# Kernel optimization log

Measured on AMD Instinct MI355X. Metric: run time of the kernel, lower is better.

The kernel has to match this reference:

```python
import jax, jax.numpy as jnp
import numpy as np

B, Q, KL, ML, D = 2, 1024, 1024, 1024, 1024
H, DK = 16, 64  # adim = H*DK = 1024
SCALE = float(np.sqrt(DK))


def _rel_shift(x):
    # x: [B, qlen, klen, H] -> TransformerXL relative shift
    b, q, k, h = x.shape
    x = jnp.pad(x, ((0, 0), (0, 0), (1, 0), (0, 0)))  # [B,q,k+1,H]
    x = x.reshape(b, k + 1, q, h)[:, 1:]               # drop first row of shifted view
    return x.reshape(b, q, k, h)


def setup_inputs() -> dict:
    key = jax.random.key(0)
    ks = jax.random.split(key, 12)
    n = lambda i, s, scale=1.0: jax.random.normal(ks[i], s, jnp.float32) * scale
    return {
        "key_x": n(0, (B, KL, D)),
        "query": n(1, (B, Q, D)),
        "memory": n(2, (B, ML, D)),
        "pos_embs": n(3, (KL + ML, 1, D)),
        "mask": jnp.ones((B, Q, KL + ML), jnp.int32),
        "u": n(4, (H, DK), 0.02),
        "v": n(5, (H, DK), 0.02),
        "w_key": n(6, (D, H * DK), 0.02),
        "w_value": n(7, (D, H * DK), 0.02),
        "w_query": n(8, (D, H * DK), 0.02),
        "w_position": n(9, (D, H * DK), 0.02),
        "w_out": n(10, (H * DK, D), 0.02),
    }


def reference(key_x, query, memory, pos_embs, mask, u, v,
              w_key, w_value, w_query, w_position, w_out):
    bs, qlen = query.shape[:2]
    kv = jnp.concatenate([memory, key_x], axis=1)          # [B, mlen+klen, D]
    klen_tot = kv.shape[1]
    val = (kv @ w_value).reshape(bs, klen_tot, H, DK)
    k = (kv @ w_key).reshape(bs, klen_tot, H, DK)
    q = (query @ w_query).reshape(bs, qlen, H, DK)
    pos = (pos_embs.reshape(-1, pos_embs.shape[-1]) @ w_position).reshape(-1, H, DK)
    AC = jnp.einsum('bihd,bjhd->bijh', q + u[None, None], k)
    BD = jnp.einsum('bihd,jhd->bijh', q + v[None, None], pos)
    BD = _rel_shift(BD)
    e = (AC + BD) / SCALE                                   # [B, q, k, H]
    neg_inf = jnp.finfo(e.dtype).min
    e = jnp.where(mask[..., None] == 0, neg_inf, e)
    aw = jax.nn.softmax(e, axis=2)
    cv = jnp.einsum('bijh,bjhd->bihd', aw, val).reshape(bs, qlen, H * DK)
    cv = cv @ w_out
    return cv, aw.transpose(0, 3, 1, 2)
```

## Files before the change

### kernel.cpp

```cpp
#include <hip/hip_runtime.h>
#include <stdint.h>

#define H 16
#define DK 64
#define QL 1024
#define KT 2048
#define DM 1024
#define BATCH 2

typedef __attribute__((ext_vector_type(4))) float f32x4;
typedef __attribute__((ext_vector_type(8))) short s16x8;

enum { EPI_K = 0, EPI_V = 1, EPI_QUV = 2, EPI_P = 3, EPI_OUT = 4 };

__device__ __forceinline__ unsigned short f2bf(float f) {
  union { float f; uint32_t u; } v; v.f = f;
  uint32_t u = v.u;
  u += 0x7fffu + ((u >> 16) & 1u);
  return (unsigned short)(u >> 16);
}
__device__ __forceinline__ float bf2f(unsigned short s) {
  union { uint32_t u; float f; } v; v.u = ((uint32_t)s) << 16;
  return v.f;
}

#define MFMA_BF16(A, B, C) __builtin_amdgcn_mfma_f32_16x16x32_bf16((A), (B), (C), 0, 0, 0)

__device__ __forceinline__ void gld_lds16(const void* g, void* l) {
  __builtin_amdgcn_global_load_lds(
      (const __attribute__((address_space(1))) void*)g,
      (__attribute__((address_space(3))) void*)l, 16, 0, 0);
}


__global__ __launch_bounds__(256) void cast_kv_kernel(
    const float* __restrict__ mem, const float* __restrict__ keyx,
    unsigned short* __restrict__ kv) {
  size_t i4 = (size_t)blockIdx.x * blockDim.x + threadIdx.x;
  if (i4 >= (size_t)BATCH * KT * DM / 4) return;
  size_t e = i4 * 4;
  int b = (int)(e >> 21);
  int rem = (int)(e & ((1u << 21) - 1));
  int j = rem >> 10;
  int d = rem & 1023;
  const float* src = (j < 1024)
      ? (mem + ((size_t)b << 20) + ((size_t)j << 10) + d)
      : (keyx + ((size_t)b << 20) + ((size_t)(j - 1024) << 10) + d);
  float4 v = *(const float4*)src;
  ushort4 o;
  o.x = f2bf(v.x); o.y = f2bf(v.y); o.z = f2bf(v.z); o.w = f2bf(v.w);
  *(ushort4*)(kv + e) = o;
}

__global__ __launch_bounds__(256) void cast4_kernel(
    const float* __restrict__ src, unsigned short* __restrict__ dst, int n4) {
  int i4 = blockIdx.x * blockDim.x + threadIdx.x;
  if (i4 >= n4) return;
  float4 v = *(const float4*)(src + (size_t)i4 * 4);
  ushort4 o;
  o.x = f2bf(v.x); o.y = f2bf(v.y); o.z = f2bf(v.z); o.w = f2bf(v.w);
  *(ushort4*)(dst + (size_t)i4 * 4) = o;
}

__global__ __launch_bounds__(256) void transpose_cast_kernel(
    const float* __restrict__ w0, const float* __restrict__ w1,
    const float* __restrict__ w2, const float* __restrict__ w3,
    const float* __restrict__ w4,
    unsigned short* __restrict__ o0, unsigned short* __restrict__ o1,
    unsigned short* __restrict__ o2, unsigned short* __restrict__ o3,
    unsigned short* __restrict__ o4) {
  __shared__ float tile[32][33];
  const float* src; unsigned short* dst;
  switch (blockIdx.z) {
    case 0: src = w0; dst = o0; break;
    case 1: src = w1; dst = o1; break;
    case 2: src = w2; dst = o2; break;
    case 3: src = w3; dst = o3; break;
    default: src = w4; dst = o4; break;
  }
  int bx = blockIdx.x * 32, by = blockIdx.y * 32;
  int tx = threadIdx.x;
  int ty = threadIdx.y;
#pragma unroll
  for (int r = 0; r < 4; ++r)
    tile[ty + r * 8][tx] = src[(size_t)(by + ty + r * 8) * DM + bx + tx];
  __syncthreads();
#pragma unroll
  for (int r = 0; r < 4; ++r)
    dst[(size_t)(bx + ty + r * 8) * DM + by + tx] = f2bf(tile[tx][ty + r * 8]);
}

__global__ __launch_bounds__(256) void pack_mask_kernel(
    const int* __restrict__ mask, unsigned long long* __restrict__ bits) {
  int t = blockIdx.x * blockDim.x + threadIdx.x;
  int wid = t >> 6, lane = t & 63;
  int v = mask[(size_t)wid * 64 + lane];
  unsigned long long bb = __ballot(v != 0);
  if (lane == 0) bits[wid] = bb;
}


__global__ __launch_bounds__(256) void gemm_nt_kernel(
    const unsigned short* __restrict__ A, const unsigned short* __restrict__ B,
    int K, int mode,
    unsigned short* __restrict__ out0, unsigned short* __restrict__ out1,
    float* __restrict__ outf,
    const float* __restrict__ uvec, const float* __restrict__ vvec) {
  __shared__ __align__(16) unsigned short lds[128 * 64 * 2];
  char* As = (char*)lds;
  char* Bs = (char*)lds + 128 * 64 * 2;

  const int tid = threadIdx.x;
  const int w = tid >> 6, lane = tid & 63;
  const int g = lane >> 4, l15 = lane & 15;
  const int m0 = blockIdx.y * 128, n0 = blockIdx.x * 128;
  const int wm = w >> 1, wn = w & 1;

  f32x4 zf = {0.f, 0.f, 0.f, 0.f};
  f32x4 acc[4][4];
#pragma unroll
  for (int a = 0; a < 4; ++a)
#pragma unroll
    for (int c = 0; c < 4; ++c) acc[a][c] = zf;

  for (int kt = 0; kt < K; kt += 64) {
#pragma unroll
    for (int q = 0; q < 4; ++q) {
      int o = (w * 4 + q) * 1024 + lane * 16;
      int row = o >> 7;
      int slot = (o & 127) >> 4;
      int ks = slot ^ (row & 7);
      gld_lds16(A + (size_t)(m0 + row) * K + kt + ks * 8, As + o);
      gld_lds16(B + (size_t)(n0 + row) * K + kt + ks * 8, Bs + o);
    }
    asm volatile("s_waitcnt vmcnt(0)" ::: "memory");
    __syncthreads();
#pragma unroll
    for (int kk = 0; kk < 2; ++kk) {
      s16x8 af[4], bfr[4];
#pragma unroll
      for (int mf = 0; mf < 4; ++mf) {
        int row = wm * 64 + mf * 16 + l15;
        af[mf] = *(const s16x8*)(As + row * 128 + ((kk * 64 + g * 16) ^ ((row & 7) << 4)));
      }
#pragma unroll
      for (int nf = 0; nf < 4; ++nf) {
        int row = wn * 64 + nf * 16 + l15;
        bfr[nf] = *(const s16x8*)(Bs + row * 128 + ((kk * 64 + g * 16) ^ ((row & 7) << 4)));
      }
#pragma unroll
      for (int mf = 0; mf < 4; ++mf)
#pragma unroll
        for (int nf = 0; nf < 4; ++nf)
          acc[mf][nf] = MFMA_BF16(af[mf], bfr[nf], acc[mf][nf]);
    }
    __syncthreads();
  }

#pragma unroll
  for (int mf = 0; mf < 4; ++mf) {
#pragma unroll
    for (int nf = 0; nf < 4; ++nf) {
#pragma unroll
      for (int i = 0; i < 4; ++i) {
        int m = m0 + wm * 64 + mf * 16 + g * 4 + i;
        int n = n0 + wn * 64 + nf * 16 + l15;
        float val = acc[mf][nf][i];
        if (mode == EPI_K) {
          int b = m >> 11, j = m & 2047, hh = n >> 6, d = n & 63;
          out0[(((size_t)(b * H + hh) * KT + j) << 6) + d] = f2bf(val);
        } else if (mode == EPI_V) {
          int hh = m >> 6, d = m & 63, b = n >> 11, j = n & 2047;
          out0[((size_t)(b * H + hh) * 64 + d) * KT + j] = f2bf(val);
        } else if (mode == EPI_QUV) {
          int b = m >> 10, i2 = m & 1023, hh = n >> 6, d = n & 63;
          size_t idx = ((size_t)(b * H + hh) * QL + i2) * 64 + d;
          out0[idx] = f2bf(val + uvec[n]);
          out1[idx] = f2bf(val + vvec[n]);
        } else if (mode == EPI_P) {
          int hh = n >> 6, d = n & 63;
          out0[(((size_t)hh * KT + m) << 6) + d] = f2bf(val);
        } else {
          outf[(size_t)m * DM + n] = val;
        }
      }
    }
  }
}


__global__ __launch_bounds__(256) void attn_kernel(
    const unsigned short* __restrict__ Qu, const unsigned short* __restrict__ Qv,
    const unsigned short* __restrict__ Kp, const unsigned short* __restrict__ Vt,
    const unsigned short* __restrict__ Pp,
    const unsigned long long* __restrict__ mbits,
    float* __restrict__ aw, unsigned short* __restrict__ cv) {
  __shared__ __align__(16) unsigned short smem[12288];
  const int w = threadIdx.x >> 6, lane = threadIdx.x & 63;
  const int g = lane >> 4, l15 = lane & 15;
  const int b = blockIdx.z, h = blockIdx.y;
  const int r0 = blockIdx.x * 64 + w * 16;
  const int bh = b * H + h;

  const unsigned short* Qu_b = Qu + (size_t)bh * QL * 64;
  const unsigned short* Qv_b = Qv + (size_t)bh * QL * 64;
  const unsigned short* Kp_b = Kp + (size_t)bh * KT * 64;
  const unsigned short* Vt_b = Vt + (size_t)bh * 64 * KT;
  const unsigned short* Pp_b = Pp + (size_t)h * KT * 64;
  float* aw_b = aw + (size_t)bh * QL * KT;
  const unsigned long long* mb_b = mbits + (size_t)b * QL * 32;

  char* ring = (char*)smem + w * 4096;
  char* plds = (char*)smem + 16384 + w * 2048;

  s16x8 zv = {0, 0, 0, 0, 0, 0, 0, 0};
  s16x8 qu[2], qv[2], qvp[2];
  {
    int r = r0 + l15;
#pragma unroll
    for (int kk = 0; kk < 2; ++kk) {
      qu[kk] = *(const s16x8*)(Qu_b + (size_t)r * 64 + kk * 32 + g * 8);
      qv[kk] = *(const s16x8*)(Qv_b + (size_t)r * 64 + kk * 32 + g * 8);
    }
    int rp = r0 + 1 + l15;
    if (rp < QL) {
#pragma unroll
      for (int kk = 0; kk < 2; ++kk)
        qvp[kk] = *(const s16x8*)(Qv_b + (size_t)rp * 64 + kk * 32 + g * 8);
    } else {
      qvp[0] = zv; qvp[1] = zv;
    }
  }

  f32x4 zf = {0.f, 0.f, 0.f, 0.f};
  const int cfirst = (1008 - r0) >> 6;

  auto compute_chunk = [&](int c) {
    const int T = c << 6;
    const bool wrap = (T >= KT);
    f32x4 bd[4];
#pragma unroll
    for (int nf = 0; nf < 4; ++nf) bd[nf] = zf;
#pragma unroll
    for (int kk = 0; kk < 2; ++kk) {
      const s16x8 a = wrap ? qvp[kk] : qv[kk];
#pragma unroll
      for (int nf = 0; nf < 4; ++nf) {
        int t = T + nf * 16 + l15;
        int prow = wrap ? (t - (KT + 1)) : t;
        s16x8 pb = zv;
        if (prow >= 0 && prow < KT)
          pb = *(const s16x8*)(Pp_b + (size_t)prow * 64 + kk * 32 + g * 8);
        bd[nf] = MFMA_BF16(a, pb, bd[nf]);
      }
    }
    char* dst = ring + (c & 1) * 2048;
#pragma unroll
    for (int nf = 0; nf < 4; ++nf)
#pragma unroll
      for (int i = 0; i < 4; ++i) {
        int rr = g * 4 + i;
        *(unsigned short*)(dst + rr * 128 + (((nf * 16 + l15) * 2) ^ ((rr & 7) << 4))) =
            f2bf(bd[nf][i]);
      }
  };

  auto step_e = [&](int s, float (&e)[4][4]) {
    const int j0 = s * 64;
    compute_chunk(cfirst + 1 + s);
    f32x4 acc[4];
#pragma unroll
    for (int nf = 0; nf < 4; ++nf) acc[nf] = zf;
#pragma unroll
    for (int kk = 0; kk < 2; ++kk) {
#pragma unroll
      for (int nf = 0; nf < 4; ++nf) {
        int j = j0 + nf * 16 + l15;
        s16x8 kb = *(const s16x8*)(Kp_b + (size_t)j * 64 + kk * 32 + g * 8);
        acc[nf] = MFMA_BF16(qu[kk], kb, acc[nf]);
      }
    }
    asm volatile("s_waitcnt lgkmcnt(0)" ::: "memory");
#pragma unroll
    for (int i = 0; i < 4; ++i) {
      int rr = g * 4 + i;
      unsigned long long mw = mb_b[(size_t)(r0 + rr) * 32 + s];
#pragma unroll
      for (int nf = 0; nf < 4; ++nf) {
        int j = j0 + nf * 16 + l15;
        int t = j + 1023 - (r0 + rr);
        float bdv = bf2f(*(const unsigned short*)(
            ring + ((t >> 6) & 1) * 2048 + rr * 128 + (((t & 63) * 2) ^ ((rr & 7) << 4))));
        float ev = (acc[nf][i] + bdv) * 0.125f;
        ev = ((mw >> (j & 63)) & 1ull) ? ev : -1e30f;
        e[nf][i] = ev;
      }
    }
  };

  float mrow[4], lrow[4];
#pragma unroll
  for (int i = 0; i < 4; ++i) { mrow[i] = -1e30f; lrow[i] = 0.f; }

  compute_chunk(cfirst);
  for (int s = 0; s < 32; ++s) {
    float e[4][4];
    step_e(s, e);
#pragma unroll
    for (int i = 0; i < 4; ++i) {
      float tmax = fmaxf(fmaxf(e[0][i], e[1][i]), fmaxf(e[2][i], e[3][i]));
#pragma unroll
      for (int d2 = 8; d2 > 0; d2 >>= 1) tmax = fmaxf(tmax, __shfl_xor(tmax, d2));
      float mnew = fmaxf(mrow[i], tmax);
      float ssum = __expf(e[0][i] - mnew) + __expf(e[1][i] - mnew) +
                   __expf(e[2][i] - mnew) + __expf(e[3][i] - mnew);
#pragma unroll
      for (int d2 = 8; d2 > 0; d2 >>= 1) ssum += __shfl_xor(ssum, d2);
      lrow[i] = lrow[i] * __expf(mrow[i] - mnew) + ssum;
      mrow[i] = mnew;
    }
  }

  f32x4 accO[4];
#pragma unroll
  for (int df = 0; df < 4; ++df) accO[df] = zf;
  float rl[4];
#pragma unroll
  for (int i = 0; i < 4; ++i) rl[i] = 1.f / lrow[i];

  compute_chunk(cfirst);
  for (int s = 0; s < 32; ++s) {
    const int j0 = s * 64;
    float e[4][4];
    step_e(s, e);
#pragma unroll
    for (int i = 0; i < 4; ++i) {
      int rr = g * 4 + i;
#pragma unroll
      for (int nf = 0; nf < 4; ++nf) {
        float p = __expf(e[nf][i] - mrow[i]) * rl[i];
        int j = j0 + nf * 16 + l15;
        aw_b[(size_t)(r0 + rr) * KT + j] = p;
        *(unsigned short*)(plds + rr * 128 + (((nf * 16 + l15) * 2) ^ ((rr & 7) << 4))) = f2bf(p);
      }
    }
    asm volatile("s_waitcnt lgkmcnt(0)" ::: "memory");
#pragma unroll
    for (int kk = 0; kk < 2; ++kk) {
      s16x8 pa = *(const s16x8*)(plds + l15 * 128 + ((kk * 64 + g * 16) ^ ((l15 & 7) << 4)));
#pragma unroll
      for (int df = 0; df < 4; ++df) {
        int d = df * 16 + l15;
        s16x8 vb = *(const s16x8*)(Vt_b + (size_t)d * KT + j0 + kk * 32 + g * 8);
        accO[df] = MFMA_BF16(pa, vb, accO[df]);
      }
    }
  }

#pragma unroll
  for (int df = 0; df < 4; ++df)
#pragma unroll
    for (int i = 0; i < 4; ++i) {
      int r = r0 + g * 4 + i;
      int d = df * 16 + l15;
      cv[((size_t)b * QL + r) * DM + h * 64 + d] = f2bf(accO[df][i]);
    }
}


extern "C" void kernel_launch(void* const* d_in, const int* in_sizes, int n_in,
                              void* d_out, int out_size, void* d_ws, size_t ws_size,
                              hipStream_t stream) {
  const float* key_x  = (const float*)d_in[0];
  const float* query  = (const float*)d_in[1];
  const float* memory = (const float*)d_in[2];
  const float* pose   = (const float*)d_in[3];
  const int*   mask   = (const int*)d_in[4];
  const float* u      = (const float*)d_in[5];
  const float* v      = (const float*)d_in[6];
  const float* w_key  = (const float*)d_in[7];
  const float* w_val  = (const float*)d_in[8];
  const float* w_qry  = (const float*)d_in[9];
  const float* w_pos  = (const float*)d_in[10];
  const float* w_out  = (const float*)d_in[11];

  char* ws = (char*)d_ws;
  const size_t MB = 1024 * 1024;
  unsigned short* kv_b  = (unsigned short*)(ws + 0);
  unsigned short* q_b   = (unsigned short*)(ws + 8 * MB);
  unsigned short* pos_b = (unsigned short*)(ws + 12 * MB);
  unsigned short* wk_t  = (unsigned short*)(ws + 16 * MB);
  unsigned short* wv_t  = (unsigned short*)(ws + 18 * MB);
  unsigned short* wq_t  = (unsigned short*)(ws + 20 * MB);
  unsigned short* wp_t  = (unsigned short*)(ws + 22 * MB);
  unsigned short* wo_t  = (unsigned short*)(ws + 24 * MB);
  unsigned short* Kp    = (unsigned short*)(ws + 26 * MB);
  unsigned short* Vt    = (unsigned short*)(ws + 34 * MB);
  unsigned short* Qu    = (unsigned short*)(ws + 42 * MB);
  unsigned short* Qv    = (unsigned short*)(ws + 46 * MB);
  unsigned short* Pp    = (unsigned short*)(ws + 50 * MB);
  unsigned short* cvb   = (unsigned short*)(ws + 54 * MB);
  unsigned long long* mb = (unsigned long long*)(ws + 58 * MB);

  float* out_cv = (float*)d_out;
  float* out_aw = (float*)d_out + (size_t)BATCH * QL * DM;

  cast_kv_kernel<<<4096, 256, 0, stream>>>(memory, key_x, kv_b);
  cast4_kernel<<<2048, 256, 0, stream>>>(query, q_b, BATCH * QL * DM / 4);
  cast4_kernel<<<2048, 256, 0, stream>>>(pose, pos_b, KT * DM / 4);
  transpose_cast_kernel<<<dim3(32, 32, 5), dim3(32, 8), 0, stream>>>(
      w_key, w_val, w_qry, w_pos, w_out, wk_t, wv_t, wq_t, wp_t, wo_t);
  pack_mask_kernel<<<16384, 256, 0, stream>>>(mask, mb);

  gemm_nt_kernel<<<dim3(8, 32), 256, 0, stream>>>(kv_b, wk_t, 1024, EPI_K, Kp, nullptr, nullptr, nullptr, nullptr);
  gemm_nt_kernel<<<dim3(32, 8), 256, 0, stream>>>(wv_t, kv_b, 1024, EPI_V, Vt, nullptr, nullptr, nullptr, nullptr);
  gemm_nt_kernel<<<dim3(8, 16), 256, 0, stream>>>(q_b, wq_t, 1024, EPI_QUV, Qu, Qv, nullptr, u, v);
  gemm_nt_kernel<<<dim3(8, 16), 256, 0, stream>>>(pos_b, wp_t, 1024, EPI_P, Pp, nullptr, nullptr, nullptr, nullptr);

  attn_kernel<<<dim3(16, 16, 2), 256, 0, stream>>>(Qu, Qv, Kp, Vt, Pp, mb, out_aw, cvb);

  gemm_nt_kernel<<<dim3(8, 16), 256, 0, stream>>>(cvb, wo_t, 1024, EPI_OUT, nullptr, nullptr, out_cv, nullptr, nullptr);
}
```

Baseline: 510.3 us.

## Split attention over key quarters into stats and output kernels with atomic reduction

Splits the single two-pass attention kernel into two kernels, each dividing the key dimension into four chunks, which gives four times as many blocks (2048 instead of 512). The first kernel computes per-chunk row max and sum and writes them out. The second merges those stats, writes the attention weights, and atomically adds partial P·V results into an fp32 buffer, which a new kernel then casts to bf16. It also packs bf16 conversions with v_cvt_pk_bf16_f32 and defers the lane-wise reductions until the end of the loop. The intent is better occupancy on the many CUs. The cost is extra launches, atomics, and reusing workspace regions: Oacc overlays kv_b and mlp overlays q_b, both of which are dead by then.

```diff
diff --git a/kernel.cpp b/kernel.cpp
--- a/kernel.cpp
+++ b/kernel.cpp
@@ -30,6 +30,17 @@
   __builtin_amdgcn_global_load_lds(
       (const __attribute__((address_space(1))) void*)g,
       (__attribute__((address_space(3))) void*)l, 16, 0, 0);
+}
+
+__device__ __forceinline__ void store_bf16_col(char* base, int g, int col2, const f32x4& v) {
+  uint32_t pk01, pk23;
+  asm("v_cvt_pk_bf16_f32 %0, %1, %2" : "=v"(pk01) : "v"(v[0]), "v"(v[1]));
+  asm("v_cvt_pk_bf16_f32 %0, %1, %2" : "=v"(pk23) : "v"(v[2]), "v"(v[3]));
+  const int rr = g * 4;
+  *(uint16_t*)(base + (rr + 0) * 128 + (col2 ^ (((rr + 0) & 7) << 4))) = (uint16_t)pk01;
+  *(uint16_t*)(base + (rr + 1) * 128 + (col2 ^ (((rr + 1) & 7) << 4))) = (uint16_t)(pk01 >> 16);
+  *(uint16_t*)(base + (rr + 2) * 128 + (col2 ^ (((rr + 2) & 7) << 4))) = (uint16_t)pk23;
+  *(uint16_t*)(base + (rr + 3) * 128 + (col2 ^ (((rr + 3) & 7) << 4))) = (uint16_t)(pk23 >> 16);
 }
 
 
@@ -189,18 +200,167 @@
 }
 
 
-__global__ __launch_bounds__(256) void attn_kernel(
+__device__ __forceinline__ void attn_chunk(
+    char* ring, const unsigned short* __restrict__ Pp_b,
+    const s16x8* qv, const s16x8* qvp, int c, int g, int l15) {
+  const int T = c << 6;
+  const bool wrap = (T >= KT);
+  const f32x4 zf = {0.f, 0.f, 0.f, 0.f};
+  const s16x8 zv = {0, 0, 0, 0, 0, 0, 0, 0};
+  f32x4 bd[4];
+#pragma unroll
+  for (int nf = 0; nf < 4; ++nf) bd[nf] = zf;
+#pragma unroll
+  for (int kk = 0; kk < 2; ++kk) {
+    const s16x8 a = wrap ? qvp[kk] : qv[kk];
+#pragma unroll
+    for (int nf = 0; nf < 4; ++nf) {
+      int t = T + nf * 16 + l15;
+      int prow = wrap ? (t - (KT + 1)) : t;
+      s16x8 pb = zv;
+      if (prow >= 0 && prow < KT)
+        pb = *(const s16x8*)(Pp_b + (size_t)prow * 64 + kk * 32 + g * 8);
+      bd[nf] = MFMA_BF16(a, pb, bd[nf]);
+    }
+  }
+  char* dst = ring + (c & 1) * 2048;
+#pragma unroll
+  for (int nf = 0; nf < 4; ++nf)
+    store_bf16_col(dst, g, (nf * 16 + l15) * 2, bd[nf]);
+}
+
+__device__ __forceinline__ void attn_step_e(
+    const unsigned short* __restrict__ Kp_b,
+    const unsigned long long* __restrict__ mb_b,
+    char* ring, const s16x8* qu,
+    int s, int r0, int g, int l15, float (&e)[4][4]) {
+  const int j0 = s * 64;
+  const f32x4 zf = {0.f, 0.f, 0.f, 0.f};
+  f32x4 acc[4];
+#pragma unroll
+  for (int nf = 0; nf < 4; ++nf) acc[nf] = zf;
+#pragma unroll
+  for (int kk = 0; kk < 2; ++kk) {
+#pragma unroll
+    for (int nf = 0; nf < 4; ++nf) {
+      int j = j0 + nf * 16 + l15;
+      s16x8 kb = *(const s16x8*)(Kp_b + (size_t)j * 64 + kk * 32 + g * 8);
+      acc[nf] = MFMA_BF16(qu[kk], kb, acc[nf]);
+    }
+  }
+  asm volatile("s_waitcnt lgkmcnt(0)" ::: "memory");
+#pragma unroll
+  for (int i = 0; i < 4; ++i) {
+    int rr = g * 4 + i;
+    unsigned long long mw = mb_b[(size_t)(r0 + rr) * 32 + s];
+#pragma unroll
+    for (int nf = 0; nf < 4; ++nf) {
+      int j = j0 + nf * 16 + l15;
+      int t = j + 1023 - (r0 + rr);
+      float bdv = bf2f(*(const unsigned short*)(
+          ring + ((t >> 6) & 1) * 2048 + rr * 128 + (((t & 63) * 2) ^ ((rr & 7) << 4))));
+      float ev = (acc[nf][i] + bdv) * 0.125f;
+      ev = ((mw >> (j & 63)) & 1ull) ? ev : -1e30f;
+      e[nf][i] = ev;
+    }
+  }
+}
+
+__global__ __launch_bounds__(256, 4) void attn_p1(
+    const unsigned short* __restrict__ Qu, const unsigned short* __restrict__ Qv,
+    const unsigned short* __restrict__ Kp, const unsigned short* __restrict__ Pp,
+    const unsigned long long* __restrict__ mbits,
+    float2* __restrict__ mlp, float* __restrict__ Oacc) {
+  __shared__ __align__(16) unsigned short smem[8192];
+  const int w = threadIdx.x >> 6, lane = threadIdx.x & 63;
+  const int g = lane >> 4, l15 = lane & 15;
+  const int bh = blockIdx.z, b = bh >> 4, h = bh & 15;
+  const int jq = blockIdx.y;
+  const int r0 = blockIdx.x * 64 + w * 16;
+
+  if (jq == 0) {
+    float4 z4 = {0.f, 0.f, 0.f, 0.f};
+    float* dst = Oacc + ((size_t)bh * QL + blockIdx.x * 64) * 64 + threadIdx.x * 16;
+#pragma unroll
+    for (int q = 0; q < 4; ++q) ((float4*)dst)[q] = z4;
+  }
+
+  const unsigned short* Qu_b = Qu + (size_t)bh * QL * 64;
+  const unsigned short* Qv_b = Qv + (size_t)bh * QL * 64;
+  const unsigned short* Kp_b = Kp + (size_t)bh * KT * 64;
+  const unsigned short* Pp_b = Pp + (size_t)h * KT * 64;
+  const unsigned long long* mb_b = mbits + (size_t)b * QL * 32;
+  char* ring = (char*)smem + w * 4096;
+
+  s16x8 zv = {0, 0, 0, 0, 0, 0, 0, 0};
+  s16x8 qu[2], qv[2], qvp[2];
+  {
+    int r = r0 + l15;
+#pragma unroll
+    for (int kk = 0; kk < 2; ++kk) {
+      qu[kk] = *(const s16x8*)(Qu_b + (size_t)r * 64 + kk * 32 + g * 8);
+      qv[kk] = *(const s16x8*)(Qv_b + (size_t)r * 64 + kk * 32 + g * 8);
+    }
+    int rp = r0 + 1 + l15;
+    if (rp < QL) {
+#pragma unroll
+      for (int kk = 0; kk < 2; ++kk)
+        qvp[kk] = *(const s16x8*)(Qv_b + (size_t)rp * 64 + kk * 32 + g * 8);
+    } else {
+      qvp[0] = zv; qvp[1] = zv;
+    }
+  }
+
+  const int cfirst = (1008 - r0) >> 6;
+  const int sq0 = jq * 8;
+
+  float m_l[4], l_l[4];
+#pragma unroll
+  for (int i = 0; i < 4; ++i) { m_l[i] = -1e30f; l_l[i] = 0.f; }
+
+  attn_chunk(ring, Pp_b, qv, qvp, cfirst + sq0, g, l15);
+  for (int s = sq0; s < sq0 + 8; ++s) {
+    attn_chunk(ring, Pp_b, qv, qvp, cfirst + 1 + s, g, l15);
+    float e[4][4];
+    attn_step_e(Kp_b, mb_b, ring, qu, s, r0, g, l15, e);
+#pragma unroll
+    for (int i = 0; i < 4; ++i) {
+      float tmax = fmaxf(fmaxf(e[0][i], e[1][i]), fmaxf(e[2][i], e[3][i]));
+      float mnew = fmaxf(m_l[i], tmax);
+      l_l[i] = l_l[i] * __expf(m_l[i] - mnew) + __expf(e[0][i] - mnew) +
+               __expf(e[1][i] - mnew) + __expf(e[2][i] - mnew) + __expf(e[3][i] - mnew);
+      m_l[i] = mnew;
+    }
+  }
+
+#pragma unroll
+  for (int i = 0; i < 4; ++i) {
+    float m_r = m_l[i];
+#pragma unroll
+    for (int d = 1; d < 16; d <<= 1) m_r = fmaxf(m_r, __shfl_xor(m_r, d));
+    float contrib = l_l[i] * __expf(m_l[i] - m_r);
+#pragma unroll
+    for (int d = 1; d < 16; d <<= 1) contrib += __shfl_xor(contrib, d);
+    if (l15 == 0) {
+      float2 p2; p2.x = m_r; p2.y = contrib;
+      mlp[((size_t)bh * QL + r0 + g * 4 + i) * 4 + jq] = p2;
+    }
+  }
+}
+
+__global__ __launch_bounds__(256, 4) void attn_p2(
     const unsigned short* __restrict__ Qu, const unsigned short* __restrict__ Qv,
     const unsigned short* __restrict__ Kp, const unsigned short* __restrict__ Vt,
     const unsigned short* __restrict__ Pp,
     const unsigned long long* __restrict__ mbits,
-    float* __restrict__ aw, unsigned short* __restrict__ cv) {
+    const float2* __restrict__ mlp,
+    float* __restrict__ aw, float* __restrict__ Oacc) {
   __shared__ __align__(16) unsigned short smem[12288];
   const int w = threadIdx.x >> 6, lane = threadIdx.x & 63;
   const int g = lane >> 4, l15 = lane & 15;
-  const int b = blockIdx.z, h = blockIdx.y;
+  const int bh = blockIdx.z, b = bh >> 4, h = bh & 15;
+  const int jq = blockIdx.y;
   const int r0 = blockIdx.x * 64 + w * 16;
-  const int bh = b * H + h;
 
   const unsigned short* Qu_b = Qu + (size_t)bh * QL * 64;
   const unsigned short* Qv_b = Qv + (size_t)bh * QL * 64;
@@ -209,9 +369,26 @@
   const unsigned short* Pp_b = Pp + (size_t)h * KT * 64;
   float* aw_b = aw + (size_t)bh * QL * KT;
   const unsigned long long* mb_b = mbits + (size_t)b * QL * 32;
-
   char* ring = (char*)smem + w * 4096;
   char* plds = (char*)smem + 16384 + w * 2048;
+
+  float m_f = -1e30f, l_f = 0.f;
+  {
+    float2 mq[4];
+#pragma unroll
+    for (int q = 0; q < 4; ++q) mq[q] = mlp[((size_t)bh * QL + r0 + l15) * 4 + q];
+#pragma unroll
+    for (int q = 0; q < 4; ++q) m_f = fmaxf(m_f, mq[q].x);
+#pragma unroll
+    for (int q = 0; q < 4; ++q) l_f += mq[q].y * __expf(mq[q].x - m_f);
+  }
+  float rl = 1.f / l_f;
+  float m_fi[4], rl_i[4];
+#pragma unroll
+  for (int i = 0; i < 4; ++i) {
+    m_fi[i] = __shfl(m_f, g * 4 + i);
+    rl_i[i] = __shfl(rl, g * 4 + i);
+  }
 
   s16x8 zv = {0, 0, 0, 0, 0, 0, 0, 0};
   s16x8 qu[2], qv[2], qvp[2];
@@ -232,117 +409,30 @@
     }
   }
 
-  f32x4 zf = {0.f, 0.f, 0.f, 0.f};
   const int cfirst = (1008 - r0) >> 6;
-
-  auto compute_chunk = [&](int c) {
-    const int T = c << 6;
-    const bool wrap = (T >= KT);
-    f32x4 bd[4];
-#pragma unroll
-    for (int nf = 0; nf < 4; ++nf) bd[nf] = zf;
-#pragma unroll
-    for (int kk = 0; kk < 2; ++kk) {
-      const s16x8 a = wrap ? qvp[kk] : qv[kk];
-#pragma unroll
-      for (int nf = 0; nf < 4; ++nf) {
-        int t = T + nf * 16 + l15;
-        int prow = wrap ? (t - (KT + 1)) : t;
-        s16x8 pb = zv;
-        if (prow >= 0 && prow < KT)
-          pb = *(const s16x8*)(Pp_b + (size_t)prow * 64 + kk * 32 + g * 8);
-        bd[nf] = MFMA_BF16(a, pb, bd[nf]);
+  const int sq0 = jq * 8;
+  const f32x4 zf = {0.f, 0.f, 0.f, 0.f};
+  f32x4 accO[4];
+#pragma unroll
+  for (int df = 0; df < 4; ++df) accO[df] = zf;
+
+  attn_chunk(ring, Pp_b, qv, qvp, cfirst + sq0, g, l15);
+  for (int s = sq0; s < sq0 + 8; ++s) {
+    const int j0 = s * 64;
+    attn_chunk(ring, Pp_b, qv, qvp, cfirst + 1 + s, g, l15);
+    float e[4][4];
+    attn_step_e(Kp_b, mb_b, ring, qu, s, r0, g, l15, e);
+#pragma unroll
+    for (int nf = 0; nf < 4; ++nf) {
+      f32x4 pv4;
+#pragma unroll
+      for (int i = 0; i < 4; ++i) {
+        float p = __expf(e[nf][i] - m_fi[i]) * rl_i[i];
+        int j = j0 + nf * 16 + l15;
+        aw_b[(size_t)(r0 + g * 4 + i) * KT + j] = p;
+        pv4[i] = p;
       }
-    }
-    char* dst = ring + (c & 1) * 2048;
-#pragma unroll
-    for (int nf = 0; nf < 4; ++nf)
-#pragma unroll
-      for (int i = 0; i < 4; ++i) {
-        int rr = g * 4 + i;
-        *(unsigned short*)(dst + rr * 128 + (((nf * 16 + l15) * 2) ^ ((rr & 7) << 4))) =
-            f2bf(bd[nf][i]);
-      }
-  };
-
-  auto step_e = [&](int s, float (&e)[4][4]) {
-    const int j0 = s * 64;
-    compute_chunk(cfirst + 1 + s);
-    f32x4 acc[4];
-#pragma unroll
-    for (int nf = 0; nf < 4; ++nf) acc[nf] = zf;
-#pragma unroll
-    for (int kk = 0; kk < 2; ++kk) {
-#pragma unroll
-      for (int nf = 0; nf < 4; ++nf) {
-        int j = j0 + nf * 16 + l15;
-        s16x8 kb = *(const s16x8*)(Kp_b + (size_t)j * 64 + kk * 32 + g * 8);
-        acc[nf] = MFMA_BF16(qu[kk], kb, acc[nf]);
-      }
-    }
-    asm volatile("s_waitcnt lgkmcnt(0)" ::: "memory");
-#pragma unroll
-    for (int i = 0; i < 4; ++i) {
-      int rr = g * 4 + i;
-      unsigned long long mw = mb_b[(size_t)(r0 + rr) * 32 + s];
-#pragma unroll
-      for (int nf = 0; nf < 4; ++nf) {
-        int j = j0 + nf * 16 + l15;
-        int t = j + 1023 - (r0 + rr);
-        float bdv = bf2f(*(const unsigned short*)(
-            ring + ((t >> 6) & 1) * 2048 + rr * 128 + (((t & 63) * 2) ^ ((rr & 7) << 4))));
-        float ev = (acc[nf][i] + bdv) * 0.125f;
-        ev = ((mw >> (j & 63)) & 1ull) ? ev : -1e30f;
-        e[nf][i] = ev;
-      }
-    }
-  };
-
-  float mrow[4], lrow[4];
-#pragma unroll
-  for (int i = 0; i < 4; ++i) { mrow[i] = -1e30f; lrow[i] = 0.f; }
-
-  compute_chunk(cfirst);
-  for (int s = 0; s < 32; ++s) {
-    float e[4][4];
-    step_e(s, e);
-#pragma unroll
-    for (int i = 0; i < 4; ++i) {
-      float tmax = fmaxf(fmaxf(e[0][i], e[1][i]), fmaxf(e[2][i], e[3][i]));
-#pragma unroll
-      for (int d2 = 8; d2 > 0; d2 >>= 1) tmax = fmaxf(tmax, __shfl_xor(tmax, d2));
-      float mnew = fmaxf(mrow[i], tmax);
-      float ssum = __expf(e[0][i] - mnew) + __expf(e[1][i] - mnew) +
-                   __expf(e[2][i] - mnew) + __expf(e[3][i] - mnew);
-#pragma unroll
-      for (int d2 = 8; d2 > 0; d2 >>= 1) ssum += __shfl_xor(ssum, d2);
-      lrow[i] = lrow[i] * __expf(mrow[i] - mnew) + ssum;
-      mrow[i] = mnew;
-    }
-  }
-
-  f32x4 accO[4];
-#pragma unroll
-  for (int df = 0; df < 4; ++df) accO[df] = zf;
-  float rl[4];
-#pragma unroll
-  for (int i = 0; i < 4; ++i) rl[i] = 1.f / lrow[i];
-
-  compute_chunk(cfirst);
-  for (int s = 0; s < 32; ++s) {
-    const int j0 = s * 64;
-    float e[4][4];
-    step_e(s, e);
-#pragma unroll
-    for (int i = 0; i < 4; ++i) {
-      int rr = g * 4 + i;
-#pragma unroll
-      for (int nf = 0; nf < 4; ++nf) {
-        float p = __expf(e[nf][i] - mrow[i]) * rl[i];
-        int j = j0 + nf * 16 + l15;
-        aw_b[(size_t)(r0 + rr) * KT + j] = p;
-        *(unsigned short*)(plds + rr * 128 + (((nf * 16 + l15) * 2) ^ ((rr & 7) << 4))) = f2bf(p);
-      }
+      store_bf16_col(plds, g, (nf * 16 + l15) * 2, pv4);
     }
     asm volatile("s_waitcnt lgkmcnt(0)" ::: "memory");
 #pragma unroll
@@ -360,11 +450,19 @@
 #pragma unroll
   for (int df = 0; df < 4; ++df)
 #pragma unroll
-    for (int i = 0; i < 4; ++i) {
-      int r = r0 + g * 4 + i;
-      int d = df * 16 + l15;
-      cv[((size_t)b * QL + r) * DM + h * 64 + d] = f2bf(accO[df][i]);
-    }
+    for (int i = 0; i < 4; ++i)
+      atomicAdd(&Oacc[((size_t)bh * QL + r0 + g * 4 + i) * 64 + df * 16 + l15], accO[df][i]);
+}
+
+__global__ __launch_bounds__(256) void cast_cv_kernel(
+    const float* __restrict__ Oacc, unsigned short* __restrict__ cvb) {
+  int t = blockIdx.x * blockDim.x + threadIdx.x;
+  int d4 = t & 15, r = (t >> 4) & 1023, bh = t >> 14;
+  int b = bh >> 4, h = bh & 15;
+  float4 v = ((const float4*)Oacc)[t];
+  ushort4 o;
+  o.x = f2bf(v.x); o.y = f2bf(v.y); o.z = f2bf(v.z); o.w = f2bf(v.w);
+  *(ushort4*)(cvb + (size_t)(b * QL + r) * DM + h * 64 + d4 * 4) = o;
 }
 
 
@@ -401,6 +499,8 @@
   unsigned short* Pp    = (unsigned short*)(ws + 50 * MB);
   unsigned short* cvb   = (unsigned short*)(ws + 54 * MB);
   unsigned long long* mb = (unsigned long long*)(ws + 58 * MB);
+  float*  Oacc = (float*)(ws + 0);
+  float2* mlp  = (float2*)(ws + 8 * MB);
 
   float* out_cv = (float*)d_out;
   float* out_aw = (float*)d_out + (size_t)BATCH * QL * DM;
@@ -417,7 +517,9 @@
   gemm_nt_kernel<<<dim3(8, 16), 256, 0, stream>>>(q_b, wq_t, 1024, EPI_QUV, Qu, Qv, nullptr, u, v);
   gemm_nt_kernel<<<dim3(8, 16), 256, 0, stream>>>(pos_b, wp_t, 1024, EPI_P, Pp, nullptr, nullptr, nullptr, nullptr);
 
-  attn_kernel<<<dim3(16, 16, 2), 256, 0, stream>>>(Qu, Qv, Kp, Vt, Pp, mb, out_aw, cvb);
+  attn_p1<<<dim3(16, 4, 32), 256, 0, stream>>>(Qu, Qv, Kp, Pp, mb, mlp, Oacc);
+  attn_p2<<<dim3(16, 4, 32), 256, 0, stream>>>(Qu, Qv, Kp, Vt, Pp, mb, mlp, out_aw, Oacc);
+  cast_cv_kernel<<<2048, 256, 0, stream>>>(Oacc, cvb);
 
   gemm_nt_kernel<<<dim3(8, 16), 256, 0, stream>>>(cvb, wo_t, 1024, EPI_OUT, nullptr, nullptr, out_cv, nullptr, nullptr);
 }
```

After: 591.2 us. 15.8% more time.
